# Kernel optimization log

Measured on AMD Instinct MI355X. Metric: run time of the kernel, lower is better.

## Reference

```python
import jax, jax.numpy as jnp
import numpy as np
import math

B, S, DIM = 2, 2048, 1024
N_HEADS, N_KV = 16, 4
HD = DIM // N_HEADS          # 64
N_REP = N_HEADS // N_KV      # 4
ROPE_THETA = 5000.0


def _rope_tables(seqlen, head_dim, theta):
    freqs = 1.0 / (theta ** (np.arange(0, head_dim, 2, dtype=np.float32) / head_dim))
    angles = np.outer(np.arange(seqlen, dtype=np.float32), freqs)  # [S, HD/2]
    return jnp.asarray(np.cos(angles)), jnp.asarray(np.sin(angles))


def setup_inputs() -> dict:
    key = jax.random.key(0)
    ks = jax.random.split(key, 6)
    x = jax.random.normal(ks[0], (B, S, DIM), dtype=jnp.float32)
    cos, sin = _rope_tables(S, HD, ROPE_THETA)
    # additive causal mask: 0 on/below diagonal, -inf above
    mask = jnp.where(jnp.tril(jnp.ones((S, S), dtype=bool)), 0.0, -jnp.inf).astype(jnp.float32)
    wq = jax.random.normal(ks[1], (DIM, N_HEADS * HD), dtype=jnp.float32) * 0.02
    wk = jax.random.normal(ks[2], (DIM, N_KV * HD), dtype=jnp.float32) * 0.02
    wv = jax.random.normal(ks[3], (DIM, N_KV * HD), dtype=jnp.float32) * 0.02
    wo = jax.random.normal(ks[4], (N_HEADS * HD, DIM), dtype=jnp.float32) * 0.02
    return {"x": x, "cos": cos, "sin": sin, "mask": mask,
            "wq": wq, "wk": wk, "wv": wv, "wo": wo}


def _apply_rope(t, cos, sin):
    # t: [B, S, H, HD]; even/odd interleaved pairs form complex numbers
    te, to = t[..., 0::2], t[..., 1::2]               # [B,S,H,HD/2]
    c = cos[None, :, None, :]
    s = sin[None, :, None, :]
    re = te * c - to * s
    im = te * s + to * c
    return jnp.stack([re, im], axis=-1).reshape(t.shape)  # re-interleave


def reference(x, cos, sin, mask, wq, wk, wv, wo):
    bsz, seqlen, _ = x.shape
    q = (x @ wq).reshape(bsz, seqlen, N_HEADS, HD)
    k = (x @ wk).reshape(bsz, seqlen, N_KV, HD)
    v = (x @ wv).reshape(bsz, seqlen, N_KV, HD)
    q = _apply_rope(q, cos, sin)
    k = _apply_rope(k, cos, sin)
    # GQA: group query heads as [kv_head g, rep r] instead of repeating K/V
    qg = q.reshape(bsz, seqlen, N_KV, N_REP, HD)
    scores = jnp.einsum('bsgrd,btgd->bgrst', qg, k) / math.sqrt(HD)  # [B,G,R,S,S]
    scores = scores + mask[None, None, None, :, :]
    p = jax.nn.softmax(scores, axis=-1)
    out = jnp.einsum('bgrst,btgd->bsgrd', p, v)       # [B,S,G,R,HD]
    out = out.reshape(bsz, seqlen, N_HEADS * HD)
    return out @ wo
```

## Files before the change

kernel.cpp:

```cpp
#include <hip/hip_runtime.h>
#include <math.h>

#define S_LEN 2048
#define B_SZ 2

typedef __bf16 bf16_8 __attribute__((ext_vector_type(8)));
typedef float  f32_4  __attribute__((ext_vector_type(4)));

__device__ __forceinline__ unsigned short ftob(float f) {
  union { __bf16 h; unsigned short u; } cv;
  cv.h = (__bf16)f;
  return cv.u;
}
__device__ __forceinline__ unsigned int pack2(float a, float b) {
  return (unsigned int)ftob(a) | ((unsigned int)ftob(b) << 16);
}

#define QSCALE (0.125f * 1.44269504f)

__device__ __forceinline__ void tr_tile(const float* __restrict__ W,
                                        unsigned short* __restrict__ Wt,
                                        int N, int bx, int by, float (*T)[33])
{
  const int k0 = by * 32, n0 = bx * 32;
  const int r = threadIdx.x >> 3, c4 = (threadIdx.x & 7) * 4;
  const float4 v = *(const float4*)&W[(size_t)(k0 + r) * N + n0 + c4];
  T[r][c4 + 0] = v.x; T[r][c4 + 1] = v.y;
  T[r][c4 + 2] = v.z; T[r][c4 + 3] = v.w;
  __syncthreads();
  ushort4 o;
  o.x = ftob(T[c4 + 0][r]); o.y = ftob(T[c4 + 1][r]);
  o.z = ftob(T[c4 + 2][r]); o.w = ftob(T[c4 + 3][r]);
  *(ushort4*)&Wt[(size_t)(n0 + r) * 1024 + k0 + c4] = o;
}

__global__ __launch_bounds__(256) void prep(
    const float* __restrict__ x, const float* __restrict__ wq,
    const float* __restrict__ wk, const float* __restrict__ wv,
    const float* __restrict__ wo,
    unsigned short* __restrict__ xb, unsigned short* __restrict__ wqkvt,
    unsigned short* __restrict__ wot)
{
  __shared__ float T[32][33];
  const int idx = blockIdx.x;
  if (idx < 1024) {
    tr_tile(wq, wqkvt, 1024, idx & 31, idx >> 5, T);
  } else if (idx < 1280) {
    const int i = idx - 1024;
    tr_tile(wk, wqkvt + 1024 * 1024, 256, i & 7, i >> 3, T);
  } else if (idx < 1536) {
    const int i = idx - 1280;
    tr_tile(wv, wqkvt + 1280 * 1024, 256, i & 7, i >> 3, T);
  } else if (idx < 2560) {
    const int i = idx - 1536;
    tr_tile(wo, wot, 1024, i & 31, i >> 5, T);
  } else {
    const int i = idx - 2560;
#pragma unroll
    for (int j = 0; j < 4; ++j) {
      const int id = i * 1024 + (int)threadIdx.x + j * 256;
      const float4 v = ((const float4*)x)[id];
      ushort4 o;
      o.x = ftob(v.x); o.y = ftob(v.y); o.z = ftob(v.z); o.w = ftob(v.w);
      ((ushort4*)xb)[id] = o;
    }
  }
}

#define GEMM_LOAD_AB(k0)                                                        \
  do {                                                                          \
    ra  = *(const uint4*)&A[(size_t)(bm + (tid >> 2)) * 1024 + (k0) + (tid & 3) * 8]; \
    rb0 = *(const uint4*)&Bt[(size_t)(bn0 * 128 + (tid >> 2)) * 1024 + (k0) + (tid & 3) * 8]; \
    rb1 = *(const uint4*)&Bt[(size_t)(bn0 * 128 + ((tid + 256) >> 2)) * 1024 + (k0) + (tid & 3) * 8]; \
  } while (0)

#define GEMM_STORE_AB()                                                         \
  do {                                                                          \
    *(uint4*)&As[tid * 8] = ra;                                                 \
    *(uint4*)&Bs[tid * 8] = rb0;                                                \
    *(uint4*)&Bs[(tid + 256) * 8] = rb1;                                        \
  } while (0)

#define GEMM_COMPUTE()                                                          \
  do {                                                                          \
    bf16_8 af[2], bf[4];                                                        \
    _Pragma("unroll")                                                           \
    for (int mt = 0; mt < 2; ++mt)                                              \
      af[mt] = *(const bf16_8*)&As[(mh + mt * 16 + l16) * 32 + quad * 8];       \
    _Pragma("unroll")                                                           \
    for (int nt = 0; nt < 4; ++nt)                                              \
      bf[nt] = *(const bf16_8*)&Bs[(nh + nt * 16 + l16) * 32 + quad * 8];       \
    _Pragma("unroll")                                                           \
    for (int mt = 0; mt < 2; ++mt)                                              \
      _Pragma("unroll")                                                         \
      for (int nt = 0; nt < 4; ++nt)                                            \
        acc[mt][nt] = __builtin_amdgcn_mfma_f32_16x16x32_bf16(af[mt], bf[nt], acc[mt][nt], 0, 0, 0); \
  } while (0)

__global__ __launch_bounds__(256) void gemm_qkv(
    const unsigned short* __restrict__ A, const unsigned short* __restrict__ Bt,
    unsigned short* __restrict__ qb, unsigned short* __restrict__ Kimg,
    unsigned short* __restrict__ Vimg,
    const float* __restrict__ cosT, const float* __restrict__ sinT)
{
  __shared__ unsigned short sm[9216];
  unsigned short* As = sm;
  unsigned short* Bs = sm + 2048;
  const int bm = blockIdx.y * 64, bn0 = blockIdx.x;
  const int tid = threadIdx.x;
  const int w = tid >> 6, lane = tid & 63, l16 = lane & 15, quad = lane >> 4;
  const int mh = (w & 1) * 32, nh = (w >> 1) * 64;

  f32_4 acc[2][4];
#pragma unroll
  for (int mt = 0; mt < 2; ++mt)
#pragma unroll
    for (int nt = 0; nt < 4; ++nt) acc[mt][nt] = (f32_4){0.f, 0.f, 0.f, 0.f};

  uint4 ra, rb0, rb1;
  GEMM_LOAD_AB(0);
  for (int i = 0; i < 32; ++i) {
    __syncthreads();
    GEMM_STORE_AB();
    if (i + 1 < 32) GEMM_LOAD_AB((i + 1) * 32);
    __syncthreads();
    GEMM_COMPUTE();
  }

  const int colbase = bn0 * 128;
  if (colbase < 1024) {
#pragma unroll
    for (int mt = 0; mt < 2; ++mt)
#pragma unroll
      for (int r = 0; r < 4; ++r) {
        const int row = bm + mh + mt * 16 + quad * 4 + r;
        const int s = row & (S_LEN - 1);
#pragma unroll
        for (int nt = 0; nt < 4; ++nt) {
          const int col = colbase + nh + nt * 16 + l16;
          float val = acc[mt][nt][r];
          const float pv = __shfl_xor(val, 1);
          const int fi = (col & 63) >> 1;
          const float cc = cosT[s * 32 + fi], ss = sinT[s * 32 + fi];
          val = (l16 & 1) ? fmaf(pv, ss, val * cc) : fmaf(val, cc, -(pv * ss));
          qb[(size_t)row * 1024 + col] = ftob(val * QSCALE);
        }
      }
  } else if (colbase < 1280) {
#pragma unroll
    for (int mt = 0; mt < 2; ++mt)
#pragma unroll
      for (int r = 0; r < 4; ++r) {
        const int row = bm + mh + mt * 16 + quad * 4 + r;
        const int s = row & (S_LEN - 1), bi = row >> 11;
        const int tile = s >> 6, key = s & 63;
#pragma unroll
        for (int nt = 0; nt < 4; ++nt) {
          const int col = colbase + nh + nt * 16 + l16;
          float val = acc[mt][nt][r];
          const float pv = __shfl_xor(val, 1);
          const int fi = (col & 63) >> 1;
          const float cc = cosT[s * 32 + fi], ss = sinT[s * 32 + fi];
          val = (l16 & 1) ? fmaf(pv, ss, val * cc) : fmaf(val, cc, -(pv * ss));
          const int gcol = col - 1024, g = gcol >> 6, d = gcol & 63;
          Kimg[(size_t)((bi * 4 + g) * 32 + tile) * 4608 + key * 72 + d] = ftob(val);
        }
      }
  } else {
    __syncthreads();
    const int half = nh >> 6;
    unsigned short* Ts = sm + half * 4608;
#pragma unroll
    for (int mt = 0; mt < 2; ++mt)
#pragma unroll
      for (int r = 0; r < 4; ++r) {
        const int key = mh + mt * 16 + quad * 4 + r;
#pragma unroll
        for (int nt = 0; nt < 4; ++nt) {
          const int d = nt * 16 + l16;
          Ts[d * 72 + key] = ftob(acc[mt][nt][r]);
        }
      }
    __syncthreads();
    const int bi = bm >> 11, tile = (bm & 2047) >> 6;
#pragma unroll
    for (int it = 0; it < 4; ++it) {
      const int c = tid + it * 256;
      const int hh = c >> 9, cc = c & 511;
      const int d = cc >> 3, k8 = (cc & 7) * 8;
      const int g = (bn0 - 10) * 2 + hh;
      const uint4 v = *(const uint4*)&sm[hh * 4608 + d * 72 + k8];
      *(uint4*)&Vimg[(size_t)((bi * 4 + g) * 32 + tile) * 4608 + d * 72 + k8] = v;
    }
  }
}

__global__ __launch_bounds__(256) void gemm_wo(
    const unsigned short* __restrict__ A, const unsigned short* __restrict__ Bt,
    float* __restrict__ C)
{
  __shared__ unsigned short sm[6144];
  unsigned short* As = sm;
  unsigned short* Bs = sm + 2048;
  const int bm = blockIdx.y * 64, bn0 = blockIdx.x;
  const int tid = threadIdx.x;
  const int w = tid >> 6, lane = tid & 63, l16 = lane & 15, quad = lane >> 4;
  const int mh = (w & 1) * 32, nh = (w >> 1) * 64;

  f32_4 acc[2][4];
#pragma unroll
  for (int mt = 0; mt < 2; ++mt)
#pragma unroll
    for (int nt = 0; nt < 4; ++nt) acc[mt][nt] = (f32_4){0.f, 0.f, 0.f, 0.f};

  uint4 ra, rb0, rb1;
  GEMM_LOAD_AB(0);
  for (int i = 0; i < 32; ++i) {
    __syncthreads();
    GEMM_STORE_AB();
    if (i + 1 < 32) GEMM_LOAD_AB((i + 1) * 32);
    __syncthreads();
    GEMM_COMPUTE();
  }
#pragma unroll
  for (int mt = 0; mt < 2; ++mt)
#pragma unroll
    for (int r = 0; r < 4; ++r) {
      const int row = bm + mh + mt * 16 + quad * 4 + r;
#pragma unroll
      for (int nt = 0; nt < 4; ++nt)
        C[(size_t)row * 1024 + bn0 * 128 + nh + nt * 16 + l16] = acc[mt][nt][r];
    }
}

__global__ __launch_bounds__(256) void flash_attn_v5(
    const unsigned short* __restrict__ Q, const unsigned short* __restrict__ Kimg,
    const unsigned short* __restrict__ Vimg, unsigned short* __restrict__ O)
{
  __shared__ unsigned short Ks[64 * 72];
  __shared__ unsigned short Vs[64 * 72];
  const int id = blockIdx.x;
  const int gb = id & 7;
  const int g = gb & 3, b = gb >> 2;
  const int j = id >> 3;
  const int qc = (j < 32) ? (63 - j) : (j - 32);
  const int tid = threadIdx.x;
  const int w = tid >> 6, lane = tid & 63, l16 = lane & 15, quad = lane >> 4;
  const int h = g * 4 + w;
  const int qbase = qc * 32;

  bf16_8 bq[2][2];
#pragma unroll
  for (int qf = 0; qf < 2; ++qf) {
    const unsigned short* qp =
        Q + ((size_t)(b * S_LEN + qbase + qf * 16 + l16)) * 1024 + h * 64;
    bq[qf][0] = *(const bf16_8*)(qp + quad * 8);
    bq[qf][1] = *(const bf16_8*)(qp + 32 + quad * 8);
  }

  f32_4 acc[2][4];
#pragma unroll
  for (int qf = 0; qf < 2; ++qf)
#pragma unroll
    for (int mt = 0; mt < 4; ++mt) acc[qf][mt] = (f32_4){0.f, 0.f, 0.f, 0.f};
  float l_part[2] = {0.f, 0.f};

  const unsigned short* kim = Kimg + (size_t)(gb * 32) * 4608;
  const unsigned short* vim = Vimg + (size_t)(gb * 32) * 4608;
  const int ntiles = (qc >> 1) + 1;

  uint4 r0, r1, r2, r3, r4;
#define FA_LOAD(t)                                                              \
  do {                                                                          \
    const unsigned short* kp = kim + (size_t)(t) * 4608;                        \
    const unsigned short* vp = vim + (size_t)(t) * 4608;                        \
    r0 = *(const uint4*)(kp + tid * 8);                                         \
    r1 = *(const uint4*)(kp + (tid + 256) * 8);                                 \
    r2 = (tid < 64) ? *(const uint4*)(kp + (tid + 512) * 8)                     \
                    : *(const uint4*)(vp + (tid - 64) * 8);                     \
    r3 = *(const uint4*)(vp + (tid + 192) * 8);                                 \
    if (tid < 128) r4 = *(const uint4*)(vp + (tid + 448) * 8);                  \
  } while (0)
#define FA_STORE()                                                              \
  do {                                                                          \
    *(uint4*)(Ks + tid * 8) = r0;                                               \
    *(uint4*)(Ks + (tid + 256) * 8) = r1;                                       \
    if (tid < 64) *(uint4*)(Ks + (tid + 512) * 8) = r2;                         \
    else          *(uint4*)(Vs + (tid - 64) * 8) = r2;                          \
    *(uint4*)(Vs + (tid + 192) * 8) = r3;                                       \
    if (tid < 128) *(uint4*)(Vs + (tid + 448) * 8) = r4;                        \
  } while (0)

  FA_LOAD(0);
  for (int tile = 0; tile < ntiles; ++tile) {
    __syncthreads();
    FA_STORE();
    if (tile + 1 < ntiles) FA_LOAD(tile + 1);
    __syncthreads();

    const bool diag = (tile == ntiles - 1);
    unsigned int pk[2][4][2];
#pragma unroll
    for (int mt = 0; mt < 4; ++mt) {
      const bf16_8 kf0 = *(const bf16_8*)&Ks[(mt * 16 + l16) * 72 + quad * 8];
      const bf16_8 kf1 = *(const bf16_8*)&Ks[(mt * 16 + l16) * 72 + 32 + quad * 8];
#pragma unroll
      for (int qf = 0; qf < 2; ++qf) {
        f32_4 z = (f32_4){0.f, 0.f, 0.f, 0.f};
        z = __builtin_amdgcn_mfma_f32_16x16x32_bf16(kf0, bq[qf][0], z, 0, 0, 0);
        z = __builtin_amdgcn_mfma_f32_16x16x32_bf16(kf1, bq[qf][1], z, 0, 0, 0);
        float p[4];
#pragma unroll
        for (int r = 0; r < 4; ++r) {
          float pv = __builtin_amdgcn_exp2f(z[r]);
          if (diag) {
            const int keyl = mt * 16 + quad * 4 + r;
            const int ql = (qc & 1) * 32 + qf * 16 + l16;
            pv = (keyl > ql) ? 0.f : pv;
          }
          l_part[qf] += pv;
          p[r] = pv;
        }
        pk[qf][mt][0] = pack2(p[0], p[1]);
        pk[qf][mt][1] = pack2(p[2], p[3]);
      }
    }
    const int srcA = (quad & 1) * 32 + l16;
    const int srcB = srcA + 16;
    const bool hiq = (quad >> 1) != 0;
    bf16_8 pfrag[2][2];
#pragma unroll
    for (int qf = 0; qf < 2; ++qf)
#pragma unroll
      for (int H = 0; H < 2; ++H) {
        const unsigned int lo0 = __shfl((int)pk[qf][2 * H][0], srcA);
        const unsigned int lo1 = __shfl((int)pk[qf][2 * H][1], srcA);
        const unsigned int lo2 = __shfl((int)pk[qf][2 * H][0], srcB);
        const unsigned int lo3 = __shfl((int)pk[qf][2 * H][1], srcB);
        const unsigned int hi0 = __shfl((int)pk[qf][2 * H + 1][0], srcA);
        const unsigned int hi1 = __shfl((int)pk[qf][2 * H + 1][1], srcA);
        const unsigned int hi2 = __shfl((int)pk[qf][2 * H + 1][0], srcB);
        const unsigned int hi3 = __shfl((int)pk[qf][2 * H + 1][1], srcB);
        uint4 u;
        u.x = hiq ? hi0 : lo0;
        u.y = hiq ? hi1 : lo1;
        u.z = hiq ? hi2 : lo2;
        u.w = hiq ? hi3 : lo3;
        pfrag[qf][H] = *(const bf16_8*)&u;
      }
#pragma unroll
    for (int mt = 0; mt < 4; ++mt) {
      const bf16_8 vf0 = *(const bf16_8*)&Vs[(mt * 16 + l16) * 72 + quad * 8];
      const bf16_8 vf1 = *(const bf16_8*)&Vs[(mt * 16 + l16) * 72 + 32 + quad * 8];
#pragma unroll
      for (int qf = 0; qf < 2; ++qf) {
        acc[qf][mt] = __builtin_amdgcn_mfma_f32_16x16x32_bf16(vf0, pfrag[qf][0], acc[qf][mt], 0, 0, 0);
        acc[qf][mt] = __builtin_amdgcn_mfma_f32_16x16x32_bf16(vf1, pfrag[qf][1], acc[qf][mt], 0, 0, 0);
      }
    }
  }

#pragma unroll
  for (int qf = 0; qf < 2; ++qf) {
    float l = l_part[qf];
    l += __shfl_xor(l, 16);
    l += __shfl_xor(l, 32);
    const float inv = 1.f / l;
    unsigned short* op =
        O + ((size_t)(b * S_LEN + qbase + qf * 16 + l16)) * 1024 + h * 64;
#pragma unroll
    for (int mt = 0; mt < 4; ++mt) {
      ushort4 ov;
#pragma unroll
      for (int r = 0; r < 4; ++r) ((unsigned short*)&ov)[r] = ftob(acc[qf][mt][r] * inv);
      *(ushort4*)&op[mt * 16 + quad * 4] = ov;
    }
  }
}

extern "C" void kernel_launch(void* const* d_in, const int* in_sizes, int n_in,
                              void* d_out, int out_size, void* d_ws, size_t ws_size,
                              hipStream_t stream)
{
  const float* x    = (const float*)d_in[0];
  const float* cosT = (const float*)d_in[1];
  const float* sinT = (const float*)d_in[2];
  const float* wq   = (const float*)d_in[4];
  const float* wk   = (const float*)d_in[5];
  const float* wv   = (const float*)d_in[6];
  const float* wo   = (const float*)d_in[7];
  float* out = (float*)d_out;

  char* ws = (char*)d_ws;
  const size_t MB = 1024 * 1024;
  unsigned short* xb    = (unsigned short*)(ws);
  unsigned short* qb    = (unsigned short*)(ws + 8 * MB);
  unsigned short* wqkvt = (unsigned short*)(ws + 16 * MB);
  unsigned short* Kimg  = (unsigned short*)(ws + 19 * MB);
  unsigned short* Vimg  = (unsigned short*)(ws + 19 * MB + 2359296);
  unsigned short* wot   = (unsigned short*)(ws + 24641536);

  prep<<<3584, 256, 0, stream>>>(x, wq, wk, wv, wo, xb, wqkvt, wot);
  gemm_qkv<<<dim3(12, 64), 256, 0, stream>>>(xb, wqkvt, qb, Kimg, Vimg, cosT, sinT);
  flash_attn_v5<<<512, 256, 0, stream>>>(qb, Kimg, Vimg, qb);
  gemm_wo<<<dim3(8, 64), 256, 0, stream>>>(qb, wot, out);
}
```

Before: 188.2 us.

## Use 128x128 GEMM tiles with direct-to-LDS loads and XOR-swizzled K/V/P layouts

Both GEMMs move from 64x128 to 128x128 block tiles and load A/B straight into shared memory with global_load_lds instead of staging through registers. K and V images drop their padding and use an XOR-swizzled 64-wide layout. The P fragment is now rebuilt in attention through a per-wave shared-memory buffer rather than many cross-lane shuffles. These changes target global-load overhead, LDS bank conflicts and shuffle cost. In exchange the GEMM loop loses its register prefetch, so loads and compute no longer overlap, and the larger tiles halve the GEMM grid.

New measurement: 183.5 us. 2.5% less time.

```diff
diff --git a/kernel.cpp b/kernel.cpp
--- a/kernel.cpp
+++ b/kernel.cpp
@@ -12,11 +12,15 @@
   cv.h = (__bf16)f;
   return cv.u;
 }
-__device__ __forceinline__ unsigned int pack2(float a, float b) {
-  return (unsigned int)ftob(a) | ((unsigned int)ftob(b) << 16);
+
+__device__ __forceinline__ void gll16(const unsigned short* g, unsigned short* l) {
+  __builtin_amdgcn_global_load_lds(
+      (const __attribute__((address_space(1))) unsigned int*)g,
+      (__attribute__((address_space(3))) unsigned int*)l, 16, 0, 0);
 }
 
 #define QSCALE (0.125f * 1.44269504f)
+
 
 __device__ __forceinline__ void tr_tile(const float* __restrict__ W,
                                         unsigned short* __restrict__ Wt,
@@ -67,35 +71,32 @@
   }
 }
 
-#define GEMM_LOAD_AB(k0)                                                        \
-  do {                                                                          \
-    ra  = *(const uint4*)&A[(size_t)(bm + (tid >> 2)) * 1024 + (k0) + (tid & 3) * 8]; \
-    rb0 = *(const uint4*)&Bt[(size_t)(bn0 * 128 + (tid >> 2)) * 1024 + (k0) + (tid & 3) * 8]; \
-    rb1 = *(const uint4*)&Bt[(size_t)(bn0 * 128 + ((tid + 256) >> 2)) * 1024 + (k0) + (tid & 3) * 8]; \
-  } while (0)
-
-#define GEMM_STORE_AB()                                                         \
-  do {                                                                          \
-    *(uint4*)&As[tid * 8] = ra;                                                 \
-    *(uint4*)&Bs[tid * 8] = rb0;                                                \
-    *(uint4*)&Bs[(tid + 256) * 8] = rb1;                                        \
-  } while (0)
-
-#define GEMM_COMPUTE()                                                          \
-  do {                                                                          \
-    bf16_8 af[2], bf[4];                                                        \
+#define G128_KLOOP(A_, B_)                                                      \
+  for (int k0 = 0; k0 < 1024; k0 += 32) {                                       \
+    __syncthreads();                                                            \
+    {                                                                           \
+      const int r = tid >> 2, o8 = (tid & 3) * 8;                               \
+      gll16(&A_[(size_t)(bm + r) * 1024 + k0 + o8], &sm[tid * 8]);              \
+      gll16(&A_[(size_t)(bm + r + 64) * 1024 + k0 + o8], &sm[(tid + 256) * 8]); \
+      gll16(&B_[(size_t)(bn0 * 128 + r) * 1024 + k0 + o8], &sm[4096 + tid * 8]);\
+      gll16(&B_[(size_t)(bn0 * 128 + r + 64) * 1024 + k0 + o8],                 \
+            &sm[4096 + (tid + 256) * 8]);                                       \
+    }                                                                           \
+    __syncthreads();                                                            \
+    bf16_8 af[4], bf[4];                                                        \
     _Pragma("unroll")                                                           \
-    for (int mt = 0; mt < 2; ++mt)                                              \
-      af[mt] = *(const bf16_8*)&As[(mh + mt * 16 + l16) * 32 + quad * 8];       \
+    for (int mt = 0; mt < 4; ++mt)                                              \
+      af[mt] = *(const bf16_8*)&sm[(mh + mt * 16 + l16) * 32 + quad * 8];       \
     _Pragma("unroll")                                                           \
     for (int nt = 0; nt < 4; ++nt)                                              \
-      bf[nt] = *(const bf16_8*)&Bs[(nh + nt * 16 + l16) * 32 + quad * 8];       \
+      bf[nt] = *(const bf16_8*)&sm[4096 + (nh + nt * 16 + l16) * 32 + quad * 8];\
     _Pragma("unroll")                                                           \
-    for (int mt = 0; mt < 2; ++mt)                                              \
+    for (int mt = 0; mt < 4; ++mt)                                              \
       _Pragma("unroll")                                                         \
       for (int nt = 0; nt < 4; ++nt)                                            \
-        acc[mt][nt] = __builtin_amdgcn_mfma_f32_16x16x32_bf16(af[mt], bf[nt], acc[mt][nt], 0, 0, 0); \
-  } while (0)
+        acc[mt][nt] = __builtin_amdgcn_mfma_f32_16x16x32_bf16(af[mt], bf[nt],   \
+                                                              acc[mt][nt], 0, 0, 0); \
+  }
 
 __global__ __launch_bounds__(256) void gemm_qkv(
     const unsigned short* __restrict__ A, const unsigned short* __restrict__ Bt,
@@ -104,33 +105,23 @@
     const float* __restrict__ cosT, const float* __restrict__ sinT)
 {
   __shared__ unsigned short sm[9216];
-  unsigned short* As = sm;
-  unsigned short* Bs = sm + 2048;
-  const int bm = blockIdx.y * 64, bn0 = blockIdx.x;
+  const int bm = blockIdx.y * 128, bn0 = blockIdx.x;
   const int tid = threadIdx.x;
   const int w = tid >> 6, lane = tid & 63, l16 = lane & 15, quad = lane >> 4;
-  const int mh = (w & 1) * 32, nh = (w >> 1) * 64;
-
-  f32_4 acc[2][4];
-#pragma unroll
-  for (int mt = 0; mt < 2; ++mt)
+  const int mh = (w & 1) * 64, nh = (w >> 1) * 64;
+
+  f32_4 acc[4][4];
+#pragma unroll
+  for (int mt = 0; mt < 4; ++mt)
 #pragma unroll
     for (int nt = 0; nt < 4; ++nt) acc[mt][nt] = (f32_4){0.f, 0.f, 0.f, 0.f};
 
-  uint4 ra, rb0, rb1;
-  GEMM_LOAD_AB(0);
-  for (int i = 0; i < 32; ++i) {
-    __syncthreads();
-    GEMM_STORE_AB();
-    if (i + 1 < 32) GEMM_LOAD_AB((i + 1) * 32);
-    __syncthreads();
-    GEMM_COMPUTE();
-  }
+  G128_KLOOP(A, Bt);
 
   const int colbase = bn0 * 128;
   if (colbase < 1024) {
 #pragma unroll
-    for (int mt = 0; mt < 2; ++mt)
+    for (int mt = 0; mt < 4; ++mt)
 #pragma unroll
       for (int r = 0; r < 4; ++r) {
         const int row = bm + mh + mt * 16 + quad * 4 + r;
@@ -148,7 +139,7 @@
       }
   } else if (colbase < 1280) {
 #pragma unroll
-    for (int mt = 0; mt < 2; ++mt)
+    for (int mt = 0; mt < 4; ++mt)
 #pragma unroll
       for (int r = 0; r < 4; ++r) {
         const int row = bm + mh + mt * 16 + quad * 4 + r;
@@ -163,34 +154,41 @@
           const float cc = cosT[s * 32 + fi], ss = sinT[s * 32 + fi];
           val = (l16 & 1) ? fmaf(pv, ss, val * cc) : fmaf(val, cc, -(pv * ss));
           const int gcol = col - 1024, g = gcol >> 6, d = gcol & 63;
-          Kimg[(size_t)((bi * 4 + g) * 32 + tile) * 4608 + key * 72 + d] = ftob(val);
+          Kimg[(size_t)((bi * 4 + g) * 32 + tile) * 4096 + key * 64 +
+               (((d >> 3) ^ (key & 7)) * 8) + (d & 7)] = ftob(val);
         }
       }
   } else {
-    __syncthreads();
-    const int half = nh >> 6;
-    unsigned short* Ts = sm + half * 4608;
-#pragma unroll
-    for (int mt = 0; mt < 2; ++mt)
-#pragma unroll
-      for (int r = 0; r < 4; ++r) {
-        const int key = mh + mt * 16 + quad * 4 + r;
-#pragma unroll
-        for (int nt = 0; nt < 4; ++nt) {
-          const int d = nt * 16 + l16;
-          Ts[d * 72 + key] = ftob(acc[mt][nt][r]);
-        }
-      }
-    __syncthreads();
-    const int bi = bm >> 11, tile = (bm & 2047) >> 6;
-#pragma unroll
-    for (int it = 0; it < 4; ++it) {
-      const int c = tid + it * 256;
-      const int hh = c >> 9, cc = c & 511;
-      const int d = cc >> 3, k8 = (cc & 7) * 8;
-      const int g = (bn0 - 10) * 2 + hh;
-      const uint4 v = *(const uint4*)&sm[hh * 4608 + d * 72 + k8];
-      *(uint4*)&Vimg[(size_t)((bi * 4 + g) * 32 + tile) * 4608 + d * 72 + k8] = v;
+    const int bi = bm >> 11, t0 = (bm & 2047) >> 6;
+    const int gp = (bn0 - 10) * 2;
+#pragma unroll
+    for (int pass = 0; pass < 2; ++pass) {
+      __syncthreads();
+      if ((w >> 1) == pass) {
+        unsigned short* Ts = sm + (w & 1) * 4608;
+#pragma unroll
+        for (int mt = 0; mt < 4; ++mt)
+#pragma unroll
+          for (int nt = 0; nt < 4; ++nt) {
+            const int keyb = mt * 16 + quad * 4;
+            const int d = nt * 16 + l16;
+            ushort4 pk;
+#pragma unroll
+            for (int r = 0; r < 4; ++r) ((unsigned short*)&pk)[r] = ftob(acc[mt][nt][r]);
+            *(ushort4*)&Ts[d * 72 + keyb] = pk;
+          }
+      }
+      __syncthreads();
+      const int g = gp + pass;
+#pragma unroll
+      for (int it = 0; it < 4; ++it) {
+        const int c = tid + it * 256;
+        const int img = c >> 9, cc = c & 511;
+        const int d = cc >> 3, ch = cc & 7;
+        const uint4 v = *(const uint4*)&sm[img * 4608 + d * 72 + ch * 8];
+        *(uint4*)&Vimg[(size_t)((bi * 4 + g) * 32 + t0 + img) * 4096 + d * 64 +
+                       ((ch ^ (d & 7)) * 8)] = v;
+      }
     }
   }
 }
@@ -199,31 +197,22 @@
     const unsigned short* __restrict__ A, const unsigned short* __restrict__ Bt,
     float* __restrict__ C)
 {
-  __shared__ unsigned short sm[6144];
-  unsigned short* As = sm;
-  unsigned short* Bs = sm + 2048;
-  const int bm = blockIdx.y * 64, bn0 = blockIdx.x;
+  __shared__ unsigned short sm[8192];
+  const int bm = blockIdx.y * 128, bn0 = blockIdx.x;
   const int tid = threadIdx.x;
   const int w = tid >> 6, lane = tid & 63, l16 = lane & 15, quad = lane >> 4;
-  const int mh = (w & 1) * 32, nh = (w >> 1) * 64;
-
-  f32_4 acc[2][4];
-#pragma unroll
-  for (int mt = 0; mt < 2; ++mt)
+  const int mh = (w & 1) * 64, nh = (w >> 1) * 64;
+
+  f32_4 acc[4][4];
+#pragma unroll
+  for (int mt = 0; mt < 4; ++mt)
 #pragma unroll
     for (int nt = 0; nt < 4; ++nt) acc[mt][nt] = (f32_4){0.f, 0.f, 0.f, 0.f};
 
-  uint4 ra, rb0, rb1;
-  GEMM_LOAD_AB(0);
-  for (int i = 0; i < 32; ++i) {
-    __syncthreads();
-    GEMM_STORE_AB();
-    if (i + 1 < 32) GEMM_LOAD_AB((i + 1) * 32);
-    __syncthreads();
-    GEMM_COMPUTE();
-  }
-#pragma unroll
-  for (int mt = 0; mt < 2; ++mt)
+  G128_KLOOP(A, Bt);
+
+#pragma unroll
+  for (int mt = 0; mt < 4; ++mt)
 #pragma unroll
     for (int r = 0; r < 4; ++r) {
       const int row = bm + mh + mt * 16 + quad * 4 + r;
@@ -233,12 +222,13 @@
     }
 }
 
-__global__ __launch_bounds__(256) void flash_attn_v5(
+__global__ __launch_bounds__(256) void flash_attn_v6(
     const unsigned short* __restrict__ Q, const unsigned short* __restrict__ Kimg,
     const unsigned short* __restrict__ Vimg, unsigned short* __restrict__ O)
 {
-  __shared__ unsigned short Ks[64 * 72];
-  __shared__ unsigned short Vs[64 * 72];
+  __shared__ unsigned short Ks[4096];
+  __shared__ unsigned short Vs[4096];
+  __shared__ unsigned short Ps[4][2048];
   const int id = blockIdx.x;
   const int gb = id & 7;
   const int g = gb & 3, b = gb >> 2;
@@ -248,6 +238,8 @@
   const int w = tid >> 6, lane = tid & 63, l16 = lane & 15, quad = lane >> 4;
   const int h = g * 4 + w;
   const int qbase = qc * 32;
+  const int swz = l16 & 7;
+  unsigned short* ps = Ps[w];
 
   bf16_8 bq[2][2];
 #pragma unroll
@@ -265,30 +257,26 @@
     for (int mt = 0; mt < 4; ++mt) acc[qf][mt] = (f32_4){0.f, 0.f, 0.f, 0.f};
   float l_part[2] = {0.f, 0.f};
 
-  const unsigned short* kim = Kimg + (size_t)(gb * 32) * 4608;
-  const unsigned short* vim = Vimg + (size_t)(gb * 32) * 4608;
+  const unsigned short* kim = Kimg + (size_t)(gb * 32) * 4096;
+  const unsigned short* vim = Vimg + (size_t)(gb * 32) * 4096;
   const int ntiles = (qc >> 1) + 1;
 
-  uint4 r0, r1, r2, r3, r4;
+  uint4 r0, r1, r2, r3;
 #define FA_LOAD(t)                                                              \
   do {                                                                          \
-    const unsigned short* kp = kim + (size_t)(t) * 4608;                        \
-    const unsigned short* vp = vim + (size_t)(t) * 4608;                        \
+    const unsigned short* kp = kim + (size_t)(t) * 4096;                        \
+    const unsigned short* vp = vim + (size_t)(t) * 4096;                        \
     r0 = *(const uint4*)(kp + tid * 8);                                         \
     r1 = *(const uint4*)(kp + (tid + 256) * 8);                                 \
-    r2 = (tid < 64) ? *(const uint4*)(kp + (tid + 512) * 8)                     \
-                    : *(const uint4*)(vp + (tid - 64) * 8);                     \
-    r3 = *(const uint4*)(vp + (tid + 192) * 8);                                 \
-    if (tid < 128) r4 = *(const uint4*)(vp + (tid + 448) * 8);                  \
+    r2 = *(const uint4*)(vp + tid * 8);                                         \
+    r3 = *(const uint4*)(vp + (tid + 256) * 8);                                 \
   } while (0)
 #define FA_STORE()                                                              \
   do {                                                                          \
     *(uint4*)(Ks + tid * 8) = r0;                                               \
     *(uint4*)(Ks + (tid + 256) * 8) = r1;                                       \
-    if (tid < 64) *(uint4*)(Ks + (tid + 512) * 8) = r2;                         \
-    else          *(uint4*)(Vs + (tid - 64) * 8) = r2;                          \
-    *(uint4*)(Vs + (tid + 192) * 8) = r3;                                       \
-    if (tid < 128) *(uint4*)(Vs + (tid + 448) * 8) = r4;                        \
+    *(uint4*)(Vs + tid * 8) = r2;                                               \
+    *(uint4*)(Vs + (tid + 256) * 8) = r3;                                       \
   } while (0)
 
   FA_LOAD(0);
@@ -299,17 +287,17 @@
     __syncthreads();
 
     const bool diag = (tile == ntiles - 1);
-    unsigned int pk[2][4][2];
 #pragma unroll
     for (int mt = 0; mt < 4; ++mt) {
-      const bf16_8 kf0 = *(const bf16_8*)&Ks[(mt * 16 + l16) * 72 + quad * 8];
-      const bf16_8 kf1 = *(const bf16_8*)&Ks[(mt * 16 + l16) * 72 + 32 + quad * 8];
+      const int krow = (mt * 16 + l16) * 64;
+      const bf16_8 kf0 = *(const bf16_8*)&Ks[krow + (quad ^ swz) * 8];
+      const bf16_8 kf1 = *(const bf16_8*)&Ks[krow + ((4 + quad) ^ swz) * 8];
 #pragma unroll
       for (int qf = 0; qf < 2; ++qf) {
         f32_4 z = (f32_4){0.f, 0.f, 0.f, 0.f};
         z = __builtin_amdgcn_mfma_f32_16x16x32_bf16(kf0, bq[qf][0], z, 0, 0, 0);
         z = __builtin_amdgcn_mfma_f32_16x16x32_bf16(kf1, bq[qf][1], z, 0, 0, 0);
-        float p[4];
+        ushort4 pk;
 #pragma unroll
         for (int r = 0; r < 4; ++r) {
           float pv = __builtin_amdgcn_exp2f(z[r]);
@@ -319,43 +307,28 @@
             pv = (keyl > ql) ? 0.f : pv;
           }
           l_part[qf] += pv;
-          p[r] = pv;
+          ((unsigned short*)&pk)[r] = ftob(pv);
         }
-        pk[qf][mt][0] = pack2(p[0], p[1]);
-        pk[qf][mt][1] = pack2(p[2], p[3]);
-      }
-    }
-    const int srcA = (quad & 1) * 32 + l16;
-    const int srcB = srcA + 16;
-    const bool hiq = (quad >> 1) != 0;
-    bf16_8 pfrag[2][2];
-#pragma unroll
-    for (int qf = 0; qf < 2; ++qf)
-#pragma unroll
-      for (int H = 0; H < 2; ++H) {
-        const unsigned int lo0 = __shfl((int)pk[qf][2 * H][0], srcA);
-        const unsigned int lo1 = __shfl((int)pk[qf][2 * H][1], srcA);
-        const unsigned int lo2 = __shfl((int)pk[qf][2 * H][0], srcB);
-        const unsigned int lo3 = __shfl((int)pk[qf][2 * H][1], srcB);
-        const unsigned int hi0 = __shfl((int)pk[qf][2 * H + 1][0], srcA);
-        const unsigned int hi1 = __shfl((int)pk[qf][2 * H + 1][1], srcA);
-        const unsigned int hi2 = __shfl((int)pk[qf][2 * H + 1][0], srcB);
-        const unsigned int hi3 = __shfl((int)pk[qf][2 * H + 1][1], srcB);
-        uint4 u;
-        u.x = hiq ? hi0 : lo0;
-        u.y = hiq ? hi1 : lo1;
-        u.z = hiq ? hi2 : lo2;
-        u.w = hiq ? hi3 : lo3;
-        pfrag[qf][H] = *(const bf16_8*)&u;
-      }
+        *(ushort4*)&ps[(qf * 16 + l16) * 64 +
+                       (((2 * mt + (quad >> 1)) ^ swz) * 8) + (quad & 1) * 4] = pk;
+      }
+    }
+    bf16_8 pf[2][2];
+#pragma unroll
+    for (int qf = 0; qf < 2; ++qf) {
+      const int prow = (qf * 16 + l16) * 64;
+      pf[qf][0] = *(const bf16_8*)&ps[prow + ((quad ^ swz) * 8)];
+      pf[qf][1] = *(const bf16_8*)&ps[prow + (((4 + quad) ^ swz) * 8)];
+    }
 #pragma unroll
     for (int mt = 0; mt < 4; ++mt) {
-      const bf16_8 vf0 = *(const bf16_8*)&Vs[(mt * 16 + l16) * 72 + quad * 8];
-      const bf16_8 vf1 = *(const bf16_8*)&Vs[(mt * 16 + l16) * 72 + 32 + quad * 8];
+      const int vrow = (mt * 16 + l16) * 64;
+      const bf16_8 vf0 = *(const bf16_8*)&Vs[vrow + (quad ^ swz) * 8];
+      const bf16_8 vf1 = *(const bf16_8*)&Vs[vrow + ((4 + quad) ^ swz) * 8];
 #pragma unroll
       for (int qf = 0; qf < 2; ++qf) {
-        acc[qf][mt] = __builtin_amdgcn_mfma_f32_16x16x32_bf16(vf0, pfrag[qf][0], acc[qf][mt], 0, 0, 0);
-        acc[qf][mt] = __builtin_amdgcn_mfma_f32_16x16x32_bf16(vf1, pfrag[qf][1], acc[qf][mt], 0, 0, 0);
+        acc[qf][mt] = __builtin_amdgcn_mfma_f32_16x16x32_bf16(vf0, pf[qf][0], acc[qf][mt], 0, 0, 0);
+        acc[qf][mt] = __builtin_amdgcn_mfma_f32_16x16x32_bf16(vf1, pf[qf][1], acc[qf][mt], 0, 0, 0);
       }
     }
   }
@@ -397,11 +370,11 @@
   unsigned short* qb    = (unsigned short*)(ws + 8 * MB);
   unsigned short* wqkvt = (unsigned short*)(ws + 16 * MB);
   unsigned short* Kimg  = (unsigned short*)(ws + 19 * MB);
-  unsigned short* Vimg  = (unsigned short*)(ws + 19 * MB + 2359296);
-  unsigned short* wot   = (unsigned short*)(ws + 24641536);
+  unsigned short* Vimg  = (unsigned short*)(ws + 21 * MB);
+  unsigned short* wot   = (unsigned short*)(ws + 23 * MB);
 
   prep<<<3584, 256, 0, stream>>>(x, wq, wk, wv, wo, xb, wqkvt, wot);
-  gemm_qkv<<<dim3(12, 64), 256, 0, stream>>>(xb, wqkvt, qb, Kimg, Vimg, cosT, sinT);
-  flash_attn_v5<<<512, 256, 0, stream>>>(qb, Kimg, Vimg, qb);
-  gemm_wo<<<dim3(8, 64), 256, 0, stream>>>(qb, wot, out);
-}
+  gemm_qkv<<<dim3(12, 32), 256, 0, stream>>>(xb, wqkvt, qb, Kimg, Vimg, cosT, sinT);
+  flash_attn_v6<<<512, 256, 0, stream>>>(qb, Kimg, Vimg, qb);
+  gemm_wo<<<dim3(8, 32), 256, 0, stream>>>(qb, wot, out);
+}
```
